# Optimization experiments

Measured on AMD Instinct MI355X. Metric: run time of the kernel, lower is better.

## Reference

```python
import jax, jax.numpy as jnp
import numpy as np

VOCAB, HID, LSTM_H, T_LEN, N_LAB, BATCH = 21128, 768, 128, 256, 9, 32


def _gru_dir(x, Wih, Whh, bih, bhh):
    # x: [B,T,D]; PyTorch GRU gate order: reset, update, new
    xp = jnp.einsum('btd,gd->tbg', x, Wih) + bih  # [T,B,3H]
    H = Whh.shape[1]
    def step(h, xt):
        gh = h @ Whh.T + bhh
        xr, xz, xn = jnp.split(xt, 3, axis=-1)
        hr, hz, hn = jnp.split(gh, 3, axis=-1)
        r = jax.nn.sigmoid(xr + hr)
        z = jax.nn.sigmoid(xz + hz)
        n = jnp.tanh(xn + r * hn)
        hnew = (1.0 - z) * n + z * h
        return hnew, hnew
    h0 = jnp.zeros((x.shape[0], H), x.dtype)
    _, hs = jax.lax.scan(step, h0, xp)
    return hs  # [T,B,H]


def _crf_llh(emissions, labels, trans, start, end):
    # emissions [B,T,L], labels [B,T]; full mask (all ones)
    e = jnp.transpose(emissions, (1, 0, 2))  # [T,B,L]
    emit_scores = jnp.take_along_axis(e, labels.T[:, :, None], axis=2)[:, :, 0]  # [T,B]
    trans_scores = trans[labels[:, :-1], labels[:, 1:]]  # [B,T-1]
    num = start[labels[:, 0]] + emit_scores.sum(0) + trans_scores.sum(1) + end[labels[:, -1]]
    def step(alpha, et):
        alpha = jax.nn.logsumexp(alpha[:, :, None] + trans[None] + et[:, None, :], axis=1)
        return alpha, None
    alpha0 = start + e[0]
    alpha, _ = jax.lax.scan(step, alpha0, e[1:])
    denom = jax.nn.logsumexp(alpha + end, axis=1)
    return num - denom  # [B]


def _viterbi(emissions, trans, start, end):
    e = jnp.transpose(emissions, (1, 0, 2))  # [T,B,L]
    def step(alpha, et):
        scores = alpha[:, :, None] + trans[None]  # [B,L_prev,L_cur]
        bp = jnp.argmax(scores, axis=1)
        alpha = jnp.max(scores, axis=1) + et
        return alpha, bp
    alpha0 = start + e[0]
    alpha, bps = jax.lax.scan(step, alpha0, e[1:])  # bps: [T-1,B,L]
    last = jnp.argmax(alpha + end, axis=1)  # [B]
    def back(y, bp):
        yprev = jnp.take_along_axis(bp, y[:, None], axis=1)[:, 0]
        return yprev, yprev
    _, path = jax.lax.scan(back, last, bps, reverse=True)  # [T-1,B]
    return jnp.concatenate([path, last[None]], axis=0).T  # [B,T]


def setup_inputs() -> dict:
    key = jax.random.key(0)
    ks = jax.random.split(key, 16)
    s = 0.02
    inp = {
        'input_ids': jax.random.randint(ks[0], (BATCH, T_LEN), 0, VOCAB),
        'attention_mask': jnp.ones((BATCH, T_LEN), jnp.int64 if jax.config.jax_enable_x64 else jnp.int32),
        'labels': jax.random.randint(ks[1], (BATCH, T_LEN), 0, N_LAB),
        'emb': jax.random.normal(ks[2], (VOCAB, HID), jnp.float32) * s,
        'Wih_f': jax.random.normal(ks[3], (3 * LSTM_H, HID), jnp.float32) * s,
        'Whh_f': jax.random.normal(ks[4], (3 * LSTM_H, LSTM_H), jnp.float32) * s,
        'bih_f': jnp.zeros((3 * LSTM_H,), jnp.float32),
        'bhh_f': jnp.zeros((3 * LSTM_H,), jnp.float32),
        'Wih_b': jax.random.normal(ks[5], (3 * LSTM_H, HID), jnp.float32) * s,
        'Whh_b': jax.random.normal(ks[6], (3 * LSTM_H, LSTM_H), jnp.float32) * s,
        'bih_b': jnp.zeros((3 * LSTM_H,), jnp.float32),
        'bhh_b': jnp.zeros((3 * LSTM_H,), jnp.float32),
        'Wlin': jax.random.normal(ks[7], (N_LAB, 2 * LSTM_H), jnp.float32) * s,
        'blin': jnp.zeros((N_LAB,), jnp.float32),
        'trans': jax.random.normal(ks[8], (N_LAB, N_LAB), jnp.float32) * 0.1,
        'start': jax.random.normal(ks[9], (N_LAB,), jnp.float32) * 0.1,
        'end': jax.random.normal(ks[10], (N_LAB,), jnp.float32) * 0.1,
    }
    return inp


def reference(input_ids, attention_mask, labels, emb, Wih_f, Whh_f, bih_f, bhh_f,
              Wih_b, Whh_b, bih_b, bhh_b, Wlin, blin, trans, start, end):
    x = emb[input_ids]  # [B,T,HID]
    hf = _gru_dir(x, Wih_f, Whh_f, bih_f, bhh_f)                 # [T,B,H]
    hb = _gru_dir(x[:, ::-1, :], Wih_b, Whh_b, bih_b, bhh_b)[::-1]  # [T,B,H]
    seq = jnp.concatenate([hf, hb], axis=-1).transpose(1, 0, 2)  # [B,T,2H]
    emissions = seq @ Wlin.T + blin                              # [B,T,L]
    decoded = _viterbi(emissions, trans, start, end)             # [B,T] int
    llh = _crf_llh(emissions, labels, trans, start, end)         # [B]
    loss = -jnp.mean(llh)
    return decoded, loss
```

## Files before the change

### kernel.cpp

```cpp
#include <hip/hip_runtime.h>
#include <math.h>

#define T_LEN 256
#define BATCH 32
#define HID   768
#define GH    384
#define LH    128
#define NLAB  9
#define M_TOT (T_LEN*BATCH)

typedef float v2f __attribute__((ext_vector_type(2)));
typedef _Float16 h8 __attribute__((ext_vector_type(8)));
typedef float f4 __attribute__((ext_vector_type(4)));

#define BC(x, i) __int_as_float(__builtin_amdgcn_ds_swizzle(__float_as_int(x), (i) << 5))

#define BAR_LGKM() do {                                   \
    asm volatile("s_waitcnt lgkmcnt(0)" ::: "memory");    \
    __builtin_amdgcn_s_barrier();                         \
    asm volatile("" ::: "memory");                        \
  } while (0)

__global__ __launch_bounds__(256, 2) void k_gemm_xp(
    const int* __restrict__ ids, const float* __restrict__ emb,
    const float* __restrict__ Wf, const float* __restrict__ Wb,
    const float* __restrict__ bihf, const float* __restrict__ bihb,
    float* __restrict__ xp)
{
  __shared__ __align__(16) _Float16 Ah[128*40];
  __shared__ __align__(16) _Float16 Bh[128*40];

  const int tid  = threadIdx.x;
  const int lane = tid & 63, w = tid >> 6;
  const int m0 = blockIdx.y * 128, n0 = blockIdx.x * 128;

  const int srow = tid >> 1, sk = (tid & 1) * 16;
  const int gm = m0 + srow;
  const int tok = ids[(gm & 31) * T_LEN + (gm >> 5)];
  const float* aG = emb + (size_t)tok * HID + sk;
  const int gn = n0 + srow;
  const float* bG = (gn < GH ? Wf + (size_t)gn * HID
                             : Wb + (size_t)(gn - GH) * HID) + sk;

  const int fr = lane & 15, fq = lane >> 4;
  const int mrow = (w & 1) * 64;
  const int ncol = (w >> 1) * 64;

  f4 acc[4][4];
#pragma unroll
  for (int i = 0; i < 4; ++i)
#pragma unroll
    for (int j = 0; j < 4; ++j) acc[i][j] = f4{0,0,0,0};

  const int sb = srow * 40 + sk;

  float4 ra[4], rb[4];
#pragma unroll
  for (int c = 0; c < 4; ++c) {
    ra[c] = *reinterpret_cast<const float4*>(aG + 4 * c);
    rb[c] = *reinterpret_cast<const float4*>(bG + 4 * c);
  }

  for (int kt = 0; kt < HID / 32; ++kt) {
    BAR_LGKM();
#pragma unroll
    for (int m = 0; m < 2; ++m) {
      const float4* src = m ? rb : ra;
      _Float16* dsth = m ? Bh : Ah;
#pragma unroll
      for (int seg = 0; seg < 2; ++seg) {
        float xs[8] = {src[2*seg].x, src[2*seg].y, src[2*seg].z, src[2*seg].w,
                       src[2*seg+1].x, src[2*seg+1].y, src[2*seg+1].z, src[2*seg+1].w};
        h8 hi;
#pragma unroll
        for (int c = 0; c < 8; ++c) hi[c] = (_Float16)xs[c];
        *reinterpret_cast<h8*>(&dsth[sb + seg * 8]) = hi;
      }
    }
    if (kt + 1 < HID / 32) {
      const float* pa = aG + (kt + 1) * 32;
      const float* pb = bG + (kt + 1) * 32;
#pragma unroll
      for (int c = 0; c < 4; ++c) {
        ra[c] = *reinterpret_cast<const float4*>(pa + 4 * c);
        rb[c] = *reinterpret_cast<const float4*>(pb + 4 * c);
      }
    }
    BAR_LGKM();

    h8 fbh[4];
#pragma unroll
    for (int j = 0; j < 4; ++j) {
      const int off = (ncol + j * 16 + fr) * 40 + fq * 8;
      fbh[j] = *reinterpret_cast<const h8*>(&Bh[off]);
    }
#pragma unroll
    for (int i = 0; i < 4; ++i) {
      const int off = (mrow + i * 16 + fr) * 40 + fq * 8;
      h8 fah = *reinterpret_cast<const h8*>(&Ah[off]);
#pragma unroll
      for (int j = 0; j < 4; ++j)
        acc[i][j] = __builtin_amdgcn_mfma_f32_16x16x32_f16(fah, fbh[j], acc[i][j], 0, 0, 0);
    }
  }

  float bcol[4];
#pragma unroll
  for (int j = 0; j < 4; ++j) {
    const int c = n0 + ncol + j * 16 + fr;
    bcol[j] = (c < GH) ? bihf[c] : bihb[c - GH];
  }
#pragma unroll
  for (int i = 0; i < 4; ++i)
#pragma unroll
    for (int j = 0; j < 4; ++j) {
      const int col = n0 + ncol + j * 16 + fr;
#pragma unroll
      for (int r = 0; r < 4; ++r) {
        const int row = m0 + mrow + i * 16 + fq * 4 + r;
        xp[(size_t)row * HID + col] = acc[i][j][r] + bcol[j];
      }
    }
}

__global__ __attribute__((amdgpu_flat_work_group_size(512, 512),
                          amdgpu_waves_per_eu(2, 2)))
void k_gru(
    const float* __restrict__ xp,
    const float* __restrict__ Whhf, const float* __restrict__ Whhb,
    const float* __restrict__ bhhf, const float* __restrict__ bhhb,
    float* __restrict__ hbuf, float* __restrict__ lossp)
{
  __shared__ __align__(1024) _Float16 hsp[2][256];
  const int tid = threadIdx.x;
  const int g   = tid >> 2;
  const int q   = tid & 3;
  const int bd  = blockIdx.x;
  const int dir = bd >> 5, b = bd & 31;
  const float* Whh = dir ? Whhb : Whhf;
  const float* bhh = dir ? bhhb : bhhf;

  if (bd == 0 && tid == 0) *lossp = 0.f;

  const float br = bhh[g], bz = bhh[g + LH], bn = bhh[g + 2*LH];
  const float* wg0 = Whh + (size_t)(0*LH + g) * LH + q * 32;
  const float* wg1 = Whh + (size_t)(1*LH + g) * LH + q * 32;
  const float* wg2 = Whh + (size_t)(2*LH + g) * LH + q * 32;

  const int t0 = dir ? (T_LEN - 1) : 0;
  const int dt = dir ? -1 : 1;
  const float* px = xp + (size_t)t0 * BATCH * HID + b * HID + dir * GH + g;
  float*       ph = hbuf + (size_t)t0 * BATCH * 256 + b * 256 + dir * LH + g;

  const long long xs = (long long)dt * BATCH * HID * 4;
  const long long hs = (long long)dt * BATCH * 256 * 4;
  const unsigned xslo = (unsigned)(xs & 0xffffffffll);
  const int      xshi = (int)(xs >> 32);
  const unsigned hslo = (unsigned)(hs & 0xffffffffll);
  const int      hshi = (int)(hs >> 32);
  const unsigned xlo = (unsigned)(uintptr_t)px, xhi = (unsigned)((uintptr_t)px >> 32);
  const unsigned hlo = (unsigned)(uintptr_t)ph, hhi = (unsigned)((uintptr_t)ph >> 32);
  const unsigned rd0 = (unsigned)(uintptr_t)(&hsp[0][q * 32]);
  const unsigned wr0 = (unsigned)(uintptr_t)(&hsp[1][g]);

  if (tid < 128) reinterpret_cast<unsigned*>(&hsp[0][0])[tid] = 0u;
  BAR_LGKM();

  int cnt = T_LEN;
  asm volatile(
    "global_load_dwordx4 v[128:131], %[wg0], off\n\t"
    "global_load_dwordx4 v[132:135], %[wg0], off offset:16\n\t"
    "global_load_dwordx4 v[136:139], %[wg0], off offset:32\n\t"
    "global_load_dwordx4 v[140:143], %[wg0], off offset:48\n\t"
    "global_load_dwordx4 v[144:147], %[wg0], off offset:64\n\t"
    "global_load_dwordx4 v[148:151], %[wg0], off offset:80\n\t"
    "global_load_dwordx4 v[152:155], %[wg0], off offset:96\n\t"
    "global_load_dwordx4 v[156:159], %[wg0], off offset:112\n\t"
    "global_load_dwordx4 v[160:163], %[wg1], off\n\t"
    "global_load_dwordx4 v[164:167], %[wg1], off offset:16\n\t"
    "global_load_dwordx4 v[168:171], %[wg1], off offset:32\n\t"
    "global_load_dwordx4 v[172:175], %[wg1], off offset:48\n\t"
    "global_load_dwordx4 v[176:179], %[wg1], off offset:64\n\t"
    "global_load_dwordx4 v[180:183], %[wg1], off offset:80\n\t"
    "global_load_dwordx4 v[184:187], %[wg1], off offset:96\n\t"
    "global_load_dwordx4 v[188:191], %[wg1], off offset:112\n\t"
    "global_load_dwordx4 v[192:195], %[wg2], off\n\t"
    "global_load_dwordx4 v[196:199], %[wg2], off offset:16\n\t"
    "global_load_dwordx4 v[200:203], %[wg2], off offset:32\n\t"
    "global_load_dwordx4 v[204:207], %[wg2], off offset:48\n\t"
    "global_load_dwordx4 v[208:211], %[wg2], off offset:64\n\t"
    "global_load_dwordx4 v[212:215], %[wg2], off offset:80\n\t"
    "global_load_dwordx4 v[216:219], %[wg2], off offset:96\n\t"
    "global_load_dwordx4 v[220:223], %[wg2], off offset:112\n\t"
    "v_mov_b32 v96, %[xlo]\n\t"
    "v_mov_b32 v97, %[xhi]\n\t"
    "v_mov_b32 v98, %[hlo]\n\t"
    "v_mov_b32 v99, %[hhi]\n\t"
    "v_mov_b32 v100, %[rd0]\n\t"
    "v_mov_b32 v101, %[wr0]\n\t"
    "global_load_dword v107, v[96:97], off\n\t"
    "global_load_dword v108, v[96:97], off offset:512\n\t"
    "global_load_dword v109, v[96:97], off offset:1024\n\t"
    "s_waitcnt vmcnt(3)\n\t"
    "v_cvt_pkrtz_f16_f32 v128, v128, v129\n\t"
    "v_cvt_pkrtz_f16_f32 v129, v130, v131\n\t"
    "v_cvt_pkrtz_f16_f32 v130, v132, v133\n\t"
    "v_cvt_pkrtz_f16_f32 v131, v134, v135\n\t"
    "v_cvt_pkrtz_f16_f32 v132, v136, v137\n\t"
    "v_cvt_pkrtz_f16_f32 v133, v138, v139\n\t"
    "v_cvt_pkrtz_f16_f32 v134, v140, v141\n\t"
    "v_cvt_pkrtz_f16_f32 v135, v142, v143\n\t"
    "v_cvt_pkrtz_f16_f32 v136, v144, v145\n\t"
    "v_cvt_pkrtz_f16_f32 v137, v146, v147\n\t"
    "v_cvt_pkrtz_f16_f32 v138, v148, v149\n\t"
    "v_cvt_pkrtz_f16_f32 v139, v150, v151\n\t"
    "v_cvt_pkrtz_f16_f32 v140, v152, v153\n\t"
    "v_cvt_pkrtz_f16_f32 v141, v154, v155\n\t"
    "v_cvt_pkrtz_f16_f32 v142, v156, v157\n\t"
    "v_cvt_pkrtz_f16_f32 v143, v158, v159\n\t"
    "v_cvt_pkrtz_f16_f32 v144, v160, v161\n\t"
    "v_cvt_pkrtz_f16_f32 v145, v162, v163\n\t"
    "v_cvt_pkrtz_f16_f32 v146, v164, v165\n\t"
    "v_cvt_pkrtz_f16_f32 v147, v166, v167\n\t"
    "v_cvt_pkrtz_f16_f32 v148, v168, v169\n\t"
    "v_cvt_pkrtz_f16_f32 v149, v170, v171\n\t"
    "v_cvt_pkrtz_f16_f32 v150, v172, v173\n\t"
    "v_cvt_pkrtz_f16_f32 v151, v174, v175\n\t"
    "v_cvt_pkrtz_f16_f32 v152, v176, v177\n\t"
    "v_cvt_pkrtz_f16_f32 v153, v178, v179\n\t"
    "v_cvt_pkrtz_f16_f32 v154, v180, v181\n\t"
    "v_cvt_pkrtz_f16_f32 v155, v182, v183\n\t"
    "v_cvt_pkrtz_f16_f32 v156, v184, v185\n\t"
    "v_cvt_pkrtz_f16_f32 v157, v186, v187\n\t"
    "v_cvt_pkrtz_f16_f32 v158, v188, v189\n\t"
    "v_cvt_pkrtz_f16_f32 v159, v190, v191\n\t"
    "v_cvt_pkrtz_f16_f32 v160, v192, v193\n\t"
    "v_cvt_pkrtz_f16_f32 v161, v194, v195\n\t"
    "v_cvt_pkrtz_f16_f32 v162, v196, v197\n\t"
    "v_cvt_pkrtz_f16_f32 v163, v198, v199\n\t"
    "v_cvt_pkrtz_f16_f32 v164, v200, v201\n\t"
    "v_cvt_pkrtz_f16_f32 v165, v202, v203\n\t"
    "v_cvt_pkrtz_f16_f32 v166, v204, v205\n\t"
    "v_cvt_pkrtz_f16_f32 v167, v206, v207\n\t"
    "v_cvt_pkrtz_f16_f32 v168, v208, v209\n\t"
    "v_cvt_pkrtz_f16_f32 v169, v210, v211\n\t"
    "v_cvt_pkrtz_f16_f32 v170, v212, v213\n\t"
    "v_cvt_pkrtz_f16_f32 v171, v214, v215\n\t"
    "v_cvt_pkrtz_f16_f32 v172, v216, v217\n\t"
    "v_cvt_pkrtz_f16_f32 v173, v218, v219\n\t"
    "v_cvt_pkrtz_f16_f32 v174, v220, v221\n\t"
    "v_cvt_pkrtz_f16_f32 v175, v222, v223\n\t"
    "v_mov_b32 v110, 0\n\t"
    "s_waitcnt vmcnt(0)\n\t"
    "0:\n\t"
    "s_waitcnt vmcnt(1)\n\t"
    "v_mov_b32 v104, v107\n\t"
    "v_mov_b32 v105, v108\n\t"
    "v_mov_b32 v106, v109\n\t"
    "ds_read_b128 v[176:179], v100\n\t"
    "ds_read_b128 v[180:183], v100 offset:16\n\t"
    "ds_read_b128 v[184:187], v100 offset:32\n\t"
    "ds_read_b128 v[188:191], v100 offset:48\n\t"
    "s_cmp_gt_u32 %[cnt], 1\n\t"
    "s_cbranch_scc0 3f\n\t"
    "v_add_co_u32 v96, vcc, %[xslo], v96\n\t"
    "v_addc_co_u32 v97, vcc, %[xshi], v97, vcc\n\t"
    "3:\n\t"
    "global_load_dword v107, v[96:97], off\n\t"
    "global_load_dword v108, v[96:97], off offset:512\n\t"
    "global_load_dword v109, v[96:97], off offset:1024\n\t"
    "s_waitcnt lgkmcnt(0)\n\t"
    "v_mov_b32 v116, 0\n\t"
    "v_mov_b32 v117, 0\n\t"
    "v_mov_b32 v118, 0\n\t"
    "v_mov_b32 v119, 0\n\t"
    "v_mov_b32 v120, 0\n\t"
    "v_mov_b32 v121, 0\n\t"
    "v_dot2_f32_f16 v116, v128, v176, v116\n\t"
    "v_dot2_f32_f16 v118, v144, v176, v118\n\t"
    "v_dot2_f32_f16 v120, v160, v176, v120\n\t"
    "v_dot2_f32_f16 v117, v129, v177, v117\n\t"
    "v_dot2_f32_f16 v119, v145, v177, v119\n\t"
    "v_dot2_f32_f16 v121, v161, v177, v121\n\t"
    "v_dot2_f32_f16 v116, v130, v178, v116\n\t"
    "v_dot2_f32_f16 v118, v146, v178, v118\n\t"
    "v_dot2_f32_f16 v120, v162, v178, v120\n\t"
    "v_dot2_f32_f16 v117, v131, v179, v117\n\t"
    "v_dot2_f32_f16 v119, v147, v179, v119\n\t"
    "v_dot2_f32_f16 v121, v163, v179, v121\n\t"
    "v_dot2_f32_f16 v116, v132, v180, v116\n\t"
    "v_dot2_f32_f16 v118, v148, v180, v118\n\t"
    "v_dot2_f32_f16 v120, v164, v180, v120\n\t"
    "v_dot2_f32_f16 v117, v133, v181, v117\n\t"
    "v_dot2_f32_f16 v119, v149, v181, v119\n\t"
    "v_dot2_f32_f16 v121, v165, v181, v121\n\t"
    "v_dot2_f32_f16 v116, v134, v182, v116\n\t"
    "v_dot2_f32_f16 v118, v150, v182, v118\n\t"
    "v_dot2_f32_f16 v120, v166, v182, v120\n\t"
    "v_dot2_f32_f16 v117, v135, v183, v117\n\t"
    "v_dot2_f32_f16 v119, v151, v183, v119\n\t"
    "v_dot2_f32_f16 v121, v167, v183, v121\n\t"
    "v_dot2_f32_f16 v116, v136, v184, v116\n\t"
    "v_dot2_f32_f16 v118, v152, v184, v118\n\t"
    "v_dot2_f32_f16 v120, v168, v184, v120\n\t"
    "v_dot2_f32_f16 v117, v137, v185, v117\n\t"
    "v_dot2_f32_f16 v119, v153, v185, v119\n\t"
    "v_dot2_f32_f16 v121, v169, v185, v121\n\t"
    "v_dot2_f32_f16 v116, v138, v186, v116\n\t"
    "v_dot2_f32_f16 v118, v154, v186, v118\n\t"
    "v_dot2_f32_f16 v120, v170, v186, v120\n\t"
    "v_dot2_f32_f16 v117, v139, v187, v117\n\t"
    "v_dot2_f32_f16 v119, v155, v187, v119\n\t"
    "v_dot2_f32_f16 v121, v171, v187, v121\n\t"
    "v_dot2_f32_f16 v116, v140, v188, v116\n\t"
    "v_dot2_f32_f16 v118, v156, v188, v118\n\t"
    "v_dot2_f32_f16 v120, v172, v188, v120\n\t"
    "v_dot2_f32_f16 v117, v141, v189, v117\n\t"
    "v_dot2_f32_f16 v119, v157, v189, v119\n\t"
    "v_dot2_f32_f16 v121, v173, v189, v121\n\t"
    "v_dot2_f32_f16 v116, v142, v190, v116\n\t"
    "v_dot2_f32_f16 v118, v158, v190, v118\n\t"
    "v_dot2_f32_f16 v120, v174, v190, v120\n\t"
    "v_dot2_f32_f16 v117, v143, v191, v117\n\t"
    "v_dot2_f32_f16 v119, v159, v191, v119\n\t"
    "v_dot2_f32_f16 v121, v175, v191, v121\n\t"
    "v_add_f32 v116, v116, v117\n\t"
    "v_add_f32 v118, v118, v119\n\t"
    "v_add_f32 v120, v120, v121\n\t"
    "s_nop 1\n\t"
    "v_add_f32 v116, v116, v116 quad_perm:[1,0,3,2] row_mask:0xf bank_mask:0xf\n\t"
    "v_add_f32 v118, v118, v118 quad_perm:[1,0,3,2] row_mask:0xf bank_mask:0xf\n\t"
    "v_add_f32 v120, v120, v120 quad_perm:[1,0,3,2] row_mask:0xf bank_mask:0xf\n\t"
    "s_nop 1\n\t"
    "v_add_f32 v116, v116, v116 quad_perm:[2,3,0,1] row_mask:0xf bank_mask:0xf\n\t"
    "v_add_f32 v118, v118, v118 quad_perm:[2,3,0,1] row_mask:0xf bank_mask:0xf\n\t"
    "v_add_f32 v120, v120, v120 quad_perm:[2,3,0,1] row_mask:0xf bank_mask:0xf\n\t"
    "s_nop 1\n\t"
    "v_add_f32 v111, v104, v116\n\t"
    "v_add_f32 v112, v105, v118\n\t"
    "v_add_f32 v113, v120, %[bn]\n\t"
    "v_add_f32 v111, v111, %[br]\n\t"
    "v_add_f32 v112, v112, %[bz]\n\t"
    "v_mul_f32 v111, 0xbfb8aa3b, v111\n\t"
    "v_mul_f32 v112, 0xbfb8aa3b, v112\n\t"
    "v_exp_f32 v111, v111\n\t"
    "v_exp_f32 v112, v112\n\t"
    "s_nop 0\n\t"
    "v_add_f32 v111, 1.0, v111\n\t"
    "v_add_f32 v112, 1.0, v112\n\t"
    "v_rcp_f32 v111, v111\n\t"
    "v_rcp_f32 v112, v112\n\t"
    "s_nop 0\n\t"
    "v_fmac_f32 v106, v111, v113\n\t"
    "v_mul_f32 v113, 0x4038aa3b, v106\n\t"
    "v_exp_f32 v113, v113\n\t"
    "v_sub_f32 v115, 1.0, v112\n\t"
    "s_nop 0\n\t"
    "v_add_f32 v114, -1.0, v113\n\t"
    "v_add_f32 v113, 1.0, v113\n\t"
    "v_rcp_f32 v113, v113\n\t"
    "s_nop 1\n\t"
    "v_mul_f32 v114, v114, v113\n\t"
    "v_mul_f32 v115, v115, v114\n\t"
    "v_fmac_f32 v115, v112, v110\n\t"
    "v_mov_b32 v110, v115\n\t"
    "v_cvt_f16_f32 v114, v115\n\t"
    "global_store_dword v[98:99], v115, off\n\t"
    "v_add_co_u32 v98, vcc, %[hslo], v98\n\t"
    "v_addc_co_u32 v99, vcc, %[hshi], v99, vcc\n\t"
    "ds_write_b16 v101, v114\n\t"
    "v_xor_b32 v100, 0x200, v100\n\t"
    "v_xor_b32 v101, 0x200, v101\n\t"
    "s_waitcnt lgkmcnt(0)\n\t"
    "s_barrier\n\t"
    "s_sub_u32 %[cnt], %[cnt], 1\n\t"
    "s_cmp_lg_u32 %[cnt], 0\n\t"
    "s_cbranch_scc1 0b\n\t"
    : [cnt]"+s"(cnt)
    : [wg0]"v"(wg0), [wg1]"v"(wg1), [wg2]"v"(wg2),
      [xlo]"v"(xlo), [xhi]"v"(xhi), [hlo]"v"(hlo), [hhi]"v"(hhi),
      [rd0]"v"(rd0), [wr0]"v"(wr0),
      [br]"v"(br), [bz]"v"(bz), [bn]"v"(bn),
      [xslo]"s"(xslo), [xshi]"v"(xshi), [hslo]"s"(hslo), [hshi]"v"(hshi)
    : "memory", "vcc", "scc",
      "v96","v97","v98","v99","v100","v101","v102","v103","v104","v105",
      "v106","v107","v108","v109","v110","v111","v112","v113","v114","v115",
      "v116","v117","v118","v119","v120","v121","v122","v123","v124","v125",
      "v126","v127","v128","v129","v130","v131","v132","v133","v134","v135",
      "v136","v137","v138","v139","v140","v141","v142","v143","v144","v145",
      "v146","v147","v148","v149","v150","v151","v152","v153","v154","v155",
      "v156","v157","v158","v159","v160","v161","v162","v163","v164","v165",
      "v166","v167","v168","v169","v170","v171","v172","v173","v174","v175",
      "v176","v177","v178","v179","v180","v181","v182","v183","v184","v185",
      "v186","v187","v188","v189","v190","v191","v192","v193","v194","v195",
      "v196","v197","v198","v199","v200","v201","v202","v203","v204","v205",
      "v206","v207","v208","v209","v210","v211","v212","v213","v214","v215",
      "v216","v217","v218","v219","v220","v221","v222","v223");
}

__global__ __launch_bounds__(256, 1) void k_crf_fused(
    const float* __restrict__ hbuf, const float* __restrict__ Wlin,
    const float* __restrict__ blin, const int* __restrict__ labels,
    const float* __restrict__ trans, const float* __restrict__ start,
    const float* __restrict__ endv, float* __restrict__ dec_out,
    float* __restrict__ lossp)
{
  __shared__ float el[T_LEN * 10];
  __shared__ __align__(16) unsigned char bp8[(T_LEN - 1) * 16];
  const int b    = blockIdx.x;
  const int tid  = threadIdx.x;
  const int lane = tid & 63, w = tid >> 6;
  const int sub  = lane >> 4, l16 = lane & 15;

  float4 wreg[NLAB][4];
#pragma unroll
  for (int j = 0; j < NLAB; ++j)
#pragma unroll
    for (int c = 0; c < 4; ++c)
      wreg[j][c] = *reinterpret_cast<const float4*>(Wlin + j * 256 + l16 * 16 + c * 4);

  for (int k = 0; k < 16; ++k) {
    const int t = w * 64 + k * 4 + sub;
    const float* hp = hbuf + ((size_t)t * BATCH + b) * 256 + l16 * 16;
    const float4 h0 = *reinterpret_cast<const float4*>(hp);
    const float4 h1 = *reinterpret_cast<const float4*>(hp + 4);
    const float4 h2 = *reinterpret_cast<const float4*>(hp + 8);
    const float4 h3 = *reinterpret_cast<const float4*>(hp + 12);
    float acc[NLAB];
#pragma unroll
    for (int j = 0; j < NLAB; ++j) {
      const float4 w0 = wreg[j][0], w1 = wreg[j][1], w2 = wreg[j][2], w3 = wreg[j][3];
      float s0 = h0.x*w0.x + h0.y*w0.y + h0.z*w0.z + h0.w*w0.w;
      float s1 = h1.x*w1.x + h1.y*w1.y + h1.z*w1.z + h1.w*w1.w;
      float s2 = h2.x*w2.x + h2.y*w2.y + h2.z*w2.z + h2.w*w2.w;
      float s3 = h3.x*w3.x + h3.y*w3.y + h3.z*w3.z + h3.w*w3.w;
      acc[j] = (s0 + s1) + (s2 + s3);
    }
#pragma unroll
    for (int j = 0; j < NLAB; ++j) {
#pragma unroll
      for (int off = 1; off < 16; off <<= 1)
        acc[j] += __shfl_xor(acc[j], off);
    }
    if (l16 < NLAB) {
      float v = acc[0];
#pragma unroll
      for (int j = 1; j < NLAB; ++j) v = (l16 == j) ? acc[j] : v;
      el[t * 10 + l16] = v + blin[l16];
    }
  }
  __syncthreads();

  if (w == 0) {
    float tcol[NLAB];
#pragma unroll
    for (int i = 0; i < NLAB; ++i)
      tcol[i] = (lane < NLAB) ? trans[i * NLAB + lane] : 0.f;
    float alpha = (lane < NLAB) ? (start[lane] + el[lane]) : -3e38f;
    float et_next = (lane < NLAB) ? el[10 + lane] : 0.f;
    for (int s = 0; s < T_LEN - 1; ++s) {
      const float et = et_next;
      if (s < T_LEN - 2)
        et_next = (lane < NLAB) ? el[(s + 2) * 10 + lane] : 0.f;
      float v[NLAB];
      v[0] = BC(alpha, 0) + tcol[0];
      v[1] = BC(alpha, 1) + tcol[1];
      v[2] = BC(alpha, 2) + tcol[2];
      v[3] = BC(alpha, 3) + tcol[3];
      v[4] = BC(alpha, 4) + tcol[4];
      v[5] = BC(alpha, 5) + tcol[5];
      v[6] = BC(alpha, 6) + tcol[6];
      v[7] = BC(alpha, 7) + tcol[7];
      v[8] = BC(alpha, 8) + tcol[8];
      float v01 = (v[0] >= v[1]) ? v[0] : v[1];  int i01 = (v[0] >= v[1]) ? 0 : 1;
      float v23 = (v[2] >= v[3]) ? v[2] : v[3];  int i23 = (v[2] >= v[3]) ? 2 : 3;
      float v45 = (v[4] >= v[5]) ? v[4] : v[5];  int i45 = (v[4] >= v[5]) ? 4 : 5;
      float v67 = (v[6] >= v[7]) ? v[6] : v[7];  int i67 = (v[6] >= v[7]) ? 6 : 7;
      float va = (v01 >= v23) ? v01 : v23;       int ia = (v01 >= v23) ? i01 : i23;
      float vb = (v45 >= v67) ? v45 : v67;       int ib = (v45 >= v67) ? i45 : i67;
      float vc = (va >= vb) ? va : vb;           int ic = (va >= vb) ? ia : ib;
      float best = (vc >= v[8]) ? vc : v[8];     int bi = (vc >= v[8]) ? ic : 8;
      alpha = best + et;
      if (lane < NLAB) bp8[s * 16 + lane] = (unsigned char)bi;
    }
    float fin = alpha + ((lane < NLAB) ? endv[lane] : 0.f);
    float fv[NLAB];
    fv[0] = BC(fin, 0); fv[1] = BC(fin, 1); fv[2] = BC(fin, 2);
    fv[3] = BC(fin, 3); fv[4] = BC(fin, 4); fv[5] = BC(fin, 5);
    fv[6] = BC(fin, 6); fv[7] = BC(fin, 7); fv[8] = BC(fin, 8);
    float f01 = (fv[0] >= fv[1]) ? fv[0] : fv[1];  int j01 = (fv[0] >= fv[1]) ? 0 : 1;
    float f23 = (fv[2] >= fv[3]) ? fv[2] : fv[3];  int j23 = (fv[2] >= fv[3]) ? 2 : 3;
    float f45 = (fv[4] >= fv[5]) ? fv[4] : fv[5];  int j45 = (fv[4] >= fv[5]) ? 4 : 5;
    float f67 = (fv[6] >= fv[7]) ? fv[6] : fv[7];  int j67 = (fv[6] >= fv[7]) ? 6 : 7;
    float fa = (f01 >= f23) ? f01 : f23;           int ja = (f01 >= f23) ? j01 : j23;
    float fb = (f45 >= f67) ? f45 : f67;           int jb = (f45 >= f67) ? j45 : j67;
    float fc = (fa >= fb) ? fa : fb;               int jc = (fa >= fb) ? ja : jb;
    int last = (fc >= fv[8]) ? jc : 8;
    if (lane == 0) {
      int y = last;
      dec_out[b * T_LEN + (T_LEN - 1)] = (float)y;
      uint4 row = *reinterpret_cast<const uint4*>(&bp8[(T_LEN - 2) * 16]);
      for (int s = T_LEN - 2; s >= 0; --s) {
        uint4 nrow = row;
        if (s > 0) nrow = *reinterpret_cast<const uint4*>(&bp8[(s - 1) * 16]);
        unsigned wsel = (y < 4) ? row.x : ((y < 8) ? row.y : row.z);
        y = (int)((wsel >> ((y & 3) * 8)) & 0xffu);
        dec_out[b * T_LEN + s] = (float)y;
        row = nrow;
      }
    }
  } else if (w == 1) {
    float tcol[NLAB];
#pragma unroll
    for (int i = 0; i < NLAB; ++i)
      tcol[i] = (lane < NLAB) ? trans[i * NLAB + lane] : 0.f;
    float ca = (lane < NLAB) ? (start[lane] + el[lane]) : -3e38f;
    float et_next = (lane < NLAB) ? el[10 + lane] : 0.f;
    for (int s = 0; s < T_LEN - 1; ++s) {
      const float et = et_next;
      if (s < T_LEN - 2)
        et_next = (lane < NLAB) ? el[(s + 2) * 10 + lane] : 0.f;
      float c[NLAB];
      c[0] = BC(ca, 0) + tcol[0];
      c[1] = BC(ca, 1) + tcol[1];
      c[2] = BC(ca, 2) + tcol[2];
      c[3] = BC(ca, 3) + tcol[3];
      c[4] = BC(ca, 4) + tcol[4];
      c[5] = BC(ca, 5) + tcol[5];
      c[6] = BC(ca, 6) + tcol[6];
      c[7] = BC(ca, 7) + tcol[7];
      c[8] = BC(ca, 8) + tcol[8];
      float m01 = fmaxf(c[0], c[1]), m23 = fmaxf(c[2], c[3]);
      float m45 = fmaxf(c[4], c[5]), m67 = fmaxf(c[6], c[7]);
      float m = fmaxf(fmaxf(fmaxf(m01, m23), fmaxf(m45, m67)), c[8]);
      float p0 = __expf(c[0]-m) + __expf(c[1]-m), p1 = __expf(c[2]-m) + __expf(c[3]-m);
      float p2 = __expf(c[4]-m) + __expf(c[5]-m), p3 = __expf(c[6]-m) + __expf(c[7]-m);
      float p = ((p0 + p1) + (p2 + p3)) + __expf(c[8]-m);
      ca = m + __logf(p) + et;
    }
    float fv[NLAB];
    fv[0] = BC(ca, 0) + endv[0];
    fv[1] = BC(ca, 1) + endv[1];
    fv[2] = BC(ca, 2) + endv[2];
    fv[3] = BC(ca, 3) + endv[3];
    fv[4] = BC(ca, 4) + endv[4];
    fv[5] = BC(ca, 5) + endv[5];
    fv[6] = BC(ca, 6) + endv[6];
    fv[7] = BC(ca, 7) + endv[7];
    fv[8] = BC(ca, 8) + endv[8];
    float mx = -3e38f;
#pragma unroll
    for (int j = 0; j < NLAB; ++j) mx = fmaxf(mx, fv[j]);
    float ps = 0.f;
#pragma unroll
    for (int j = 0; j < NLAB; ++j) ps += __expf(fv[j] - mx);
    float denom = mx + __logf(ps);

    const int* lb = labels + b * T_LEN;
    float part = 0.f;
    for (int t4 = 0; t4 < 4; ++t4) {
      int t = lane * 4 + t4;
      int l = lb[t];
      part += el[t * 10 + l];
      if (t > 0) part += trans[lb[t - 1] * NLAB + l];
    }
#pragma unroll
    for (int off = 32; off > 0; off >>= 1) part += __shfl_xor(part, off);
    if (lane == 0) {
      float num = part + start[lb[0]] + endv[lb[T_LEN - 1]];
      float llh = num - denom;
      atomicAdd(lossp, -llh * (1.0f / BATCH));
    }
  }
}

extern "C" void kernel_launch(void* const* d_in, const int* in_sizes, int n_in,
                              void* d_out, int out_size, void* d_ws, size_t ws_size,
                              hipStream_t stream) {
  const int*   ids    = (const int*)d_in[0];
  const int*   labels = (const int*)d_in[2];
  const float* emb    = (const float*)d_in[3];
  const float* Wihf   = (const float*)d_in[4];
  const float* Whhf   = (const float*)d_in[5];
  const float* bihf   = (const float*)d_in[6];
  const float* bhhf   = (const float*)d_in[7];
  const float* Wihb   = (const float*)d_in[8];
  const float* Whhb   = (const float*)d_in[9];
  const float* bihb   = (const float*)d_in[10];
  const float* bhhb   = (const float*)d_in[11];
  const float* Wlin   = (const float*)d_in[12];
  const float* blin   = (const float*)d_in[13];
  const float* trans  = (const float*)d_in[14];
  const float* start  = (const float*)d_in[15];
  const float* endv   = (const float*)d_in[16];

  float* xp    = (float*)d_ws;
  float* hbuf  = xp + (size_t)M_TOT * HID;
  float* out   = (float*)d_out;
  float* lossp = out + M_TOT;

  k_gemm_xp<<<dim3(6, 64), 256, 0, stream>>>(ids, emb, Wihf, Wihb, bihf, bihb, xp);
  k_gru<<<64, 512, 0, stream>>>(xp, Whhf, Whhb, bhhf, bhhb, hbuf, lossp);
  k_crf_fused<<<BATCH, 256, 0, stream>>>(hbuf, Wlin, blin, labels, trans,
                                         start, endv, out, lossp);
}
```

Measured before the change: 360.0 us.

## Split GRU hidden-row dot products across two lanes instead of four

The recurrent GRU kernel now uses 256 threads per block, with two lanes per hidden unit, each holding 64 columns of the three Whh gate rows in fp16 registers instead of 32. Each lane reads 128 bytes of h from LDS per step and one cross-lane DPP reduction stage is removed. The aim is to shorten the per-timestep critical path by using fewer waves, fewer barrier participants and a shallower reduction. The cost is twice the dot-product work per lane and a register footprint that reaches v255.

After: 355.1 us. About the same (-1.4%).

```diff
diff --git a/kernel.cpp b/kernel.cpp
--- a/kernel.cpp
+++ b/kernel.cpp
@@ -123,8 +123,8 @@
     }
 }
 
-__global__ __attribute__((amdgpu_flat_work_group_size(512, 512),
-                          amdgpu_waves_per_eu(2, 2)))
+__global__ __attribute__((amdgpu_flat_work_group_size(256, 256),
+                          amdgpu_waves_per_eu(1, 1)))
 void k_gru(
     const float* __restrict__ xp,
     const float* __restrict__ Whhf, const float* __restrict__ Whhb,
@@ -133,8 +133,8 @@
 {
   __shared__ __align__(1024) _Float16 hsp[2][256];
   const int tid = threadIdx.x;
-  const int g   = tid >> 2;
-  const int q   = tid & 3;
+  const int g   = tid >> 1;
+  const int hf  = tid & 1;
   const int bd  = blockIdx.x;
   const int dir = bd >> 5, b = bd & 31;
   const float* Whh = dir ? Whhb : Whhf;
@@ -143,9 +143,9 @@
   if (bd == 0 && tid == 0) *lossp = 0.f;
 
   const float br = bhh[g], bz = bhh[g + LH], bn = bhh[g + 2*LH];
-  const float* wg0 = Whh + (size_t)(0*LH + g) * LH + q * 32;
-  const float* wg1 = Whh + (size_t)(1*LH + g) * LH + q * 32;
-  const float* wg2 = Whh + (size_t)(2*LH + g) * LH + q * 32;
+  const float* wg0 = Whh + (size_t)(0*LH + g) * LH + hf * 64;
+  const float* wg1 = Whh + (size_t)(1*LH + g) * LH + hf * 64;
+  const float* wg2 = Whh + (size_t)(2*LH + g) * LH + hf * 64;
 
   const int t0 = dir ? (T_LEN - 1) : 0;
   const int dt = dir ? -1 : 1;
@@ -160,7 +160,7 @@
   const int      hshi = (int)(hs >> 32);
   const unsigned xlo = (unsigned)(uintptr_t)px, xhi = (unsigned)((uintptr_t)px >> 32);
   const unsigned hlo = (unsigned)(uintptr_t)ph, hhi = (unsigned)((uintptr_t)ph >> 32);
-  const unsigned rd0 = (unsigned)(uintptr_t)(&hsp[0][q * 32]);
+  const unsigned rd0 = (unsigned)(uintptr_t)(&hsp[0][hf * 64]);
   const unsigned wr0 = (unsigned)(uintptr_t)(&hsp[1][g]);
 
   if (tid < 128) reinterpret_cast<unsigned*>(&hsp[0][0])[tid] = 0u;
@@ -176,32 +176,37 @@
     "global_load_dwordx4 v[148:151], %[wg0], off offset:80\n\t"
     "global_load_dwordx4 v[152:155], %[wg0], off offset:96\n\t"
     "global_load_dwordx4 v[156:159], %[wg0], off offset:112\n\t"
-    "global_load_dwordx4 v[160:163], %[wg1], off\n\t"
-    "global_load_dwordx4 v[164:167], %[wg1], off offset:16\n\t"
-    "global_load_dwordx4 v[168:171], %[wg1], off offset:32\n\t"
-    "global_load_dwordx4 v[172:175], %[wg1], off offset:48\n\t"
-    "global_load_dwordx4 v[176:179], %[wg1], off offset:64\n\t"
-    "global_load_dwordx4 v[180:183], %[wg1], off offset:80\n\t"
-    "global_load_dwordx4 v[184:187], %[wg1], off offset:96\n\t"
-    "global_load_dwordx4 v[188:191], %[wg1], off offset:112\n\t"
-    "global_load_dwordx4 v[192:195], %[wg2], off\n\t"
-    "global_load_dwordx4 v[196:199], %[wg2], off offset:16\n\t"
-    "global_load_dwordx4 v[200:203], %[wg2], off offset:32\n\t"
-    "global_load_dwordx4 v[204:207], %[wg2], off offset:48\n\t"
-    "global_load_dwordx4 v[208:211], %[wg2], off offset:64\n\t"
-    "global_load_dwordx4 v[212:215], %[wg2], off offset:80\n\t"
-    "global_load_dwordx4 v[216:219], %[wg2], off offset:96\n\t"
-    "global_load_dwordx4 v[220:223], %[wg2], off offset:112\n\t"
+    "global_load_dwordx4 v[160:163], %[wg0], off offset:128\n\t"
+    "global_load_dwordx4 v[164:167], %[wg0], off offset:144\n\t"
+    "global_load_dwordx4 v[168:171], %[wg0], off offset:160\n\t"
+    "global_load_dwordx4 v[172:175], %[wg0], off offset:176\n\t"
+    "global_load_dwordx4 v[176:179], %[wg0], off offset:192\n\t"
+    "global_load_dwordx4 v[180:183], %[wg0], off offset:208\n\t"
+    "global_load_dwordx4 v[184:187], %[wg0], off offset:224\n\t"
+    "global_load_dwordx4 v[188:191], %[wg0], off offset:240\n\t"
+    "global_load_dwordx4 v[192:195], %[wg1], off\n\t"
+    "global_load_dwordx4 v[196:199], %[wg1], off offset:16\n\t"
+    "global_load_dwordx4 v[200:203], %[wg1], off offset:32\n\t"
+    "global_load_dwordx4 v[204:207], %[wg1], off offset:48\n\t"
+    "global_load_dwordx4 v[208:211], %[wg1], off offset:64\n\t"
+    "global_load_dwordx4 v[212:215], %[wg1], off offset:80\n\t"
+    "global_load_dwordx4 v[216:219], %[wg1], off offset:96\n\t"
+    "global_load_dwordx4 v[220:223], %[wg1], off offset:112\n\t"
+    "global_load_dwordx4 v[224:227], %[wg1], off offset:128\n\t"
+    "global_load_dwordx4 v[228:231], %[wg1], off offset:144\n\t"
+    "global_load_dwordx4 v[232:235], %[wg1], off offset:160\n\t"
+    "global_load_dwordx4 v[236:239], %[wg1], off offset:176\n\t"
+    "global_load_dwordx4 v[240:243], %[wg1], off offset:192\n\t"
+    "global_load_dwordx4 v[244:247], %[wg1], off offset:208\n\t"
+    "global_load_dwordx4 v[248:251], %[wg1], off offset:224\n\t"
+    "global_load_dwordx4 v[252:255], %[wg1], off offset:240\n\t"
     "v_mov_b32 v96, %[xlo]\n\t"
     "v_mov_b32 v97, %[xhi]\n\t"
     "v_mov_b32 v98, %[hlo]\n\t"
     "v_mov_b32 v99, %[hhi]\n\t"
     "v_mov_b32 v100, %[rd0]\n\t"
     "v_mov_b32 v101, %[wr0]\n\t"
-    "global_load_dword v107, v[96:97], off\n\t"
-    "global_load_dword v108, v[96:97], off offset:512\n\t"
-    "global_load_dword v109, v[96:97], off offset:1024\n\t"
-    "s_waitcnt vmcnt(3)\n\t"
+    "s_waitcnt vmcnt(0)\n\t"
     "v_cvt_pkrtz_f16_f32 v128, v128, v129\n\t"
     "v_cvt_pkrtz_f16_f32 v129, v130, v131\n\t"
     "v_cvt_pkrtz_f16_f32 v130, v132, v133\n\t"
@@ -250,6 +255,74 @@
     "v_cvt_pkrtz_f16_f32 v173, v218, v219\n\t"
     "v_cvt_pkrtz_f16_f32 v174, v220, v221\n\t"
     "v_cvt_pkrtz_f16_f32 v175, v222, v223\n\t"
+    "v_cvt_pkrtz_f16_f32 v176, v224, v225\n\t"
+    "v_cvt_pkrtz_f16_f32 v177, v226, v227\n\t"
+    "v_cvt_pkrtz_f16_f32 v178, v228, v229\n\t"
+    "v_cvt_pkrtz_f16_f32 v179, v230, v231\n\t"
+    "v_cvt_pkrtz_f16_f32 v180, v232, v233\n\t"
+    "v_cvt_pkrtz_f16_f32 v181, v234, v235\n\t"
+    "v_cvt_pkrtz_f16_f32 v182, v236, v237\n\t"
+    "v_cvt_pkrtz_f16_f32 v183, v238, v239\n\t"
+    "v_cvt_pkrtz_f16_f32 v184, v240, v241\n\t"
+    "v_cvt_pkrtz_f16_f32 v185, v242, v243\n\t"
+    "v_cvt_pkrtz_f16_f32 v186, v244, v245\n\t"
+    "v_cvt_pkrtz_f16_f32 v187, v246, v247\n\t"
+    "v_cvt_pkrtz_f16_f32 v188, v248, v249\n\t"
+    "v_cvt_pkrtz_f16_f32 v189, v250, v251\n\t"
+    "v_cvt_pkrtz_f16_f32 v190, v252, v253\n\t"
+    "v_cvt_pkrtz_f16_f32 v191, v254, v255\n\t"
+    "global_load_dwordx4 v[192:195], %[wg2], off\n\t"
+    "global_load_dwordx4 v[196:199], %[wg2], off offset:16\n\t"
+    "global_load_dwordx4 v[200:203], %[wg2], off offset:32\n\t"
+    "global_load_dwordx4 v[204:207], %[wg2], off offset:48\n\t"
+    "global_load_dwordx4 v[208:211], %[wg2], off offset:64\n\t"
+    "global_load_dwordx4 v[212:215], %[wg2], off offset:80\n\t"
+    "global_load_dwordx4 v[216:219], %[wg2], off offset:96\n\t"
+    "global_load_dwordx4 v[220:223], %[wg2], off offset:112\n\t"
+    "global_load_dwordx4 v[224:227], %[wg2], off offset:128\n\t"
+    "global_load_dwordx4 v[228:231], %[wg2], off offset:144\n\t"
+    "global_load_dwordx4 v[232:235], %[wg2], off offset:160\n\t"
+    "global_load_dwordx4 v[236:239], %[wg2], off offset:176\n\t"
+    "global_load_dwordx4 v[240:243], %[wg2], off offset:192\n\t"
+    "global_load_dwordx4 v[244:247], %[wg2], off offset:208\n\t"
+    "global_load_dwordx4 v[248:251], %[wg2], off offset:224\n\t"
+    "global_load_dwordx4 v[252:255], %[wg2], off offset:240\n\t"
+    "global_load_dword v107, v[96:97], off\n\t"
+    "global_load_dword v108, v[96:97], off offset:512\n\t"
+    "global_load_dword v109, v[96:97], off offset:1024\n\t"
+    "s_waitcnt vmcnt(3)\n\t"
+    "v_cvt_pkrtz_f16_f32 v192, v192, v193\n\t"
+    "v_cvt_pkrtz_f16_f32 v193, v194, v195\n\t"
+    "v_cvt_pkrtz_f16_f32 v194, v196, v197\n\t"
+    "v_cvt_pkrtz_f16_f32 v195, v198, v199\n\t"
+    "v_cvt_pkrtz_f16_f32 v196, v200, v201\n\t"
+    "v_cvt_pkrtz_f16_f32 v197, v202, v203\n\t"
+    "v_cvt_pkrtz_f16_f32 v198, v204, v205\n\t"
+    "v_cvt_pkrtz_f16_f32 v199, v206, v207\n\t"
+    "v_cvt_pkrtz_f16_f32 v200, v208, v209\n\t"
+    "v_cvt_pkrtz_f16_f32 v201, v210, v211\n\t"
+    "v_cvt_pkrtz_f16_f32 v202, v212, v213\n\t"
+    "v_cvt_pkrtz_f16_f32 v203, v214, v215\n\t"
+    "v_cvt_pkrtz_f16_f32 v204, v216, v217\n\t"
+    "v_cvt_pkrtz_f16_f32 v205, v218, v219\n\t"
+    "v_cvt_pkrtz_f16_f32 v206, v220, v221\n\t"
+    "v_cvt_pkrtz_f16_f32 v207, v222, v223\n\t"
+    "v_cvt_pkrtz_f16_f32 v208, v224, v225\n\t"
+    "v_cvt_pkrtz_f16_f32 v209, v226, v227\n\t"
+    "v_cvt_pkrtz_f16_f32 v210, v228, v229\n\t"
+    "v_cvt_pkrtz_f16_f32 v211, v230, v231\n\t"
+    "v_cvt_pkrtz_f16_f32 v212, v232, v233\n\t"
+    "v_cvt_pkrtz_f16_f32 v213, v234, v235\n\t"
+    "v_cvt_pkrtz_f16_f32 v214, v236, v237\n\t"
+    "v_cvt_pkrtz_f16_f32 v215, v238, v239\n\t"
+    "v_cvt_pkrtz_f16_f32 v216, v240, v241\n\t"
+    "v_cvt_pkrtz_f16_f32 v217, v242, v243\n\t"
+    "v_cvt_pkrtz_f16_f32 v218, v244, v245\n\t"
+    "v_cvt_pkrtz_f16_f32 v219, v246, v247\n\t"
+    "v_cvt_pkrtz_f16_f32 v220, v248, v249\n\t"
+    "v_cvt_pkrtz_f16_f32 v221, v250, v251\n\t"
+    "v_cvt_pkrtz_f16_f32 v222, v252, v253\n\t"
+    "v_cvt_pkrtz_f16_f32 v223, v254, v255\n\t"
     "v_mov_b32 v110, 0\n\t"
     "s_waitcnt vmcnt(0)\n\t"
     "0:\n\t"
@@ -257,10 +330,14 @@
     "v_mov_b32 v104, v107\n\t"
     "v_mov_b32 v105, v108\n\t"
     "v_mov_b32 v106, v109\n\t"
-    "ds_read_b128 v[176:179], v100\n\t"
-    "ds_read_b128 v[180:183], v100 offset:16\n\t"
-    "ds_read_b128 v[184:187], v100 offset:32\n\t"
-    "ds_read_b128 v[188:191], v100 offset:48\n\t"
+    "ds_read_b128 v[224:227], v100\n\t"
+    "ds_read_b128 v[228:231], v100 offset:16\n\t"
+    "ds_read_b128 v[232:235], v100 offset:32\n\t"
+    "ds_read_b128 v[236:239], v100 offset:48\n\t"
+    "ds_read_b128 v[240:243], v100 offset:64\n\t"
+    "ds_read_b128 v[244:247], v100 offset:80\n\t"
+    "ds_read_b128 v[248:251], v100 offset:96\n\t"
+    "ds_read_b128 v[252:255], v100 offset:112\n\t"
     "s_cmp_gt_u32 %[cnt], 1\n\t"
     "s_cbranch_scc0 3f\n\t"
     "v_add_co_u32 v96, vcc, %[xslo], v96\n\t"
@@ -276,54 +353,102 @@
     "v_mov_b32 v119, 0\n\t"
     "v_mov_b32 v120, 0\n\t"
     "v_mov_b32 v121, 0\n\t"
-    "v_dot2_f32_f16 v116, v128, v176, v116\n\t"
-    "v_dot2_f32_f16 v118, v144, v176, v118\n\t"
-    "v_dot2_f32_f16 v120, v160, v176, v120\n\t"
-    "v_dot2_f32_f16 v117, v129, v177, v117\n\t"
-    "v_dot2_f32_f16 v119, v145, v177, v119\n\t"
-    "v_dot2_f32_f16 v121, v161, v177, v121\n\t"
-    "v_dot2_f32_f16 v116, v130, v178, v116\n\t"
-    "v_dot2_f32_f16 v118, v146, v178, v118\n\t"
-    "v_dot2_f32_f16 v120, v162, v178, v120\n\t"
-    "v_dot2_f32_f16 v117, v131, v179, v117\n\t"
-    "v_dot2_f32_f16 v119, v147, v179, v119\n\t"
-    "v_dot2_f32_f16 v121, v163, v179, v121\n\t"
-    "v_dot2_f32_f16 v116, v132, v180, v116\n\t"
-    "v_dot2_f32_f16 v118, v148, v180, v118\n\t"
-    "v_dot2_f32_f16 v120, v164, v180, v120\n\t"
-    "v_dot2_f32_f16 v117, v133, v181, v117\n\t"
-    "v_dot2_f32_f16 v119, v149, v181, v119\n\t"
-    "v_dot2_f32_f16 v121, v165, v181, v121\n\t"
-    "v_dot2_f32_f16 v116, v134, v182, v116\n\t"
-    "v_dot2_f32_f16 v118, v150, v182, v118\n\t"
-    "v_dot2_f32_f16 v120, v166, v182, v120\n\t"
-    "v_dot2_f32_f16 v117, v135, v183, v117\n\t"
-    "v_dot2_f32_f16 v119, v151, v183, v119\n\t"
-    "v_dot2_f32_f16 v121, v167, v183, v121\n\t"
-    "v_dot2_f32_f16 v116, v136, v184, v116\n\t"
-    "v_dot2_f32_f16 v118, v152, v184, v118\n\t"
-    "v_dot2_f32_f16 v120, v168, v184, v120\n\t"
-    "v_dot2_f32_f16 v117, v137, v185, v117\n\t"
-    "v_dot2_f32_f16 v119, v153, v185, v119\n\t"
-    "v_dot2_f32_f16 v121, v169, v185, v121\n\t"
-    "v_dot2_f32_f16 v116, v138, v186, v116\n\t"
-    "v_dot2_f32_f16 v118, v154, v186, v118\n\t"
-    "v_dot2_f32_f16 v120, v170, v186, v120\n\t"
-    "v_dot2_f32_f16 v117, v139, v187, v117\n\t"
-    "v_dot2_f32_f16 v119, v155, v187, v119\n\t"
-    "v_dot2_f32_f16 v121, v171, v187, v121\n\t"
-    "v_dot2_f32_f16 v116, v140, v188, v116\n\t"
-    "v_dot2_f32_f16 v118, v156, v188, v118\n\t"
-    "v_dot2_f32_f16 v120, v172, v188, v120\n\t"
-    "v_dot2_f32_f16 v117, v141, v189, v117\n\t"
-    "v_dot2_f32_f16 v119, v157, v189, v119\n\t"
-    "v_dot2_f32_f16 v121, v173, v189, v121\n\t"
-    "v_dot2_f32_f16 v116, v142, v190, v116\n\t"
-    "v_dot2_f32_f16 v118, v158, v190, v118\n\t"
-    "v_dot2_f32_f16 v120, v174, v190, v120\n\t"
-    "v_dot2_f32_f16 v117, v143, v191, v117\n\t"
-    "v_dot2_f32_f16 v119, v159, v191, v119\n\t"
-    "v_dot2_f32_f16 v121, v175, v191, v121\n\t"
+    "v_dot2_f32_f16 v116, v128, v224, v116\n\t"
+    "v_dot2_f32_f16 v118, v160, v224, v118\n\t"
+    "v_dot2_f32_f16 v120, v192, v224, v120\n\t"
+    "v_dot2_f32_f16 v117, v129, v225, v117\n\t"
+    "v_dot2_f32_f16 v119, v161, v225, v119\n\t"
+    "v_dot2_f32_f16 v121, v193, v225, v121\n\t"
+    "v_dot2_f32_f16 v116, v130, v226, v116\n\t"
+    "v_dot2_f32_f16 v118, v162, v226, v118\n\t"
+    "v_dot2_f32_f16 v120, v194, v226, v120\n\t"
+    "v_dot2_f32_f16 v117, v131, v227, v117\n\t"
+    "v_dot2_f32_f16 v119, v163, v227, v119\n\t"
+    "v_dot2_f32_f16 v121, v195, v227, v121\n\t"
+    "v_dot2_f32_f16 v116, v132, v228, v116\n\t"
+    "v_dot2_f32_f16 v118, v164, v228, v118\n\t"
+    "v_dot2_f32_f16 v120, v196, v228, v120\n\t"
+    "v_dot2_f32_f16 v117, v133, v229, v117\n\t"
+    "v_dot2_f32_f16 v119, v165, v229, v119\n\t"
+    "v_dot2_f32_f16 v121, v197, v229, v121\n\t"
+    "v_dot2_f32_f16 v116, v134, v230, v116\n\t"
+    "v_dot2_f32_f16 v118, v166, v230, v118\n\t"
+    "v_dot2_f32_f16 v120, v198, v230, v120\n\t"
+    "v_dot2_f32_f16 v117, v135, v231, v117\n\t"
+    "v_dot2_f32_f16 v119, v167, v231, v119\n\t"
+    "v_dot2_f32_f16 v121, v199, v231, v121\n\t"
+    "v_dot2_f32_f16 v116, v136, v232, v116\n\t"
+    "v_dot2_f32_f16 v118, v168, v232, v118\n\t"
+    "v_dot2_f32_f16 v120, v200, v232, v120\n\t"
+    "v_dot2_f32_f16 v117, v137, v233, v117\n\t"
+    "v_dot2_f32_f16 v119, v169, v233, v119\n\t"
+    "v_dot2_f32_f16 v121, v201, v233, v121\n\t"
+    "v_dot2_f32_f16 v116, v138, v234, v116\n\t"
+    "v_dot2_f32_f16 v118, v170, v234, v118\n\t"
+    "v_dot2_f32_f16 v120, v202, v234, v120\n\t"
+    "v_dot2_f32_f16 v117, v139, v235, v117\n\t"
+    "v_dot2_f32_f16 v119, v171, v235, v119\n\t"
+    "v_dot2_f32_f16 v121, v203, v235, v121\n\t"
+    "v_dot2_f32_f16 v116, v140, v236, v116\n\t"
+    "v_dot2_f32_f16 v118, v172, v236, v118\n\t"
+    "v_dot2_f32_f16 v120, v204, v236, v120\n\t"
+    "v_dot2_f32_f16 v117, v141, v237, v117\n\t"
+    "v_dot2_f32_f16 v119, v173, v237, v119\n\t"
+    "v_dot2_f32_f16 v121, v205, v237, v121\n\t"
+    "v_dot2_f32_f16 v116, v142, v238, v116\n\t"
+    "v_dot2_f32_f16 v118, v174, v238, v118\n\t"
+    "v_dot2_f32_f16 v120, v206, v238, v120\n\t"
+    "v_dot2_f32_f16 v117, v143, v239, v117\n\t"
+    "v_dot2_f32_f16 v119, v175, v239, v119\n\t"
+    "v_dot2_f32_f16 v121, v207, v239, v121\n\t"
+    "v_dot2_f32_f16 v116, v144, v240, v116\n\t"
+    "v_dot2_f32_f16 v118, v176, v240, v118\n\t"
+    "v_dot2_f32_f16 v120, v208, v240, v120\n\t"
+    "v_dot2_f32_f16 v117, v145, v241, v117\n\t"
+    "v_dot2_f32_f16 v119, v177, v241, v119\n\t"
+    "v_dot2_f32_f16 v121, v209, v241, v121\n\t"
+    "v_dot2_f32_f16 v116, v146, v242, v116\n\t"
+    "v_dot2_f32_f16 v118, v178, v242, v118\n\t"
+    "v_dot2_f32_f16 v120, v210, v242, v120\n\t"
+    "v_dot2_f32_f16 v117, v147, v243, v117\n\t"
+    "v_dot2_f32_f16 v119, v179, v243, v119\n\t"
+    "v_dot2_f32_f16 v121, v211, v243, v121\n\t"
+    "v_dot2_f32_f16 v116, v148, v244, v116\n\t"
+    "v_dot2_f32_f16 v118, v180, v244, v118\n\t"
+    "v_dot2_f32_f16 v120, v212, v244, v120\n\t"
+    "v_dot2_f32_f16 v117, v149, v245, v117\n\t"
+    "v_dot2_f32_f16 v119, v181, v245, v119\n\t"
+    "v_dot2_f32_f16 v121, v213, v245, v121\n\t"
+    "v_dot2_f32_f16 v116, v150, v246, v116\n\t"
+    "v_dot2_f32_f16 v118, v182, v246, v118\n\t"
+    "v_dot2_f32_f16 v120, v214, v246, v120\n\t"
+    "v_dot2_f32_f16 v117, v151, v247, v117\n\t"
+    "v_dot2_f32_f16 v119, v183, v247, v119\n\t"
+    "v_dot2_f32_f16 v121, v215, v247, v121\n\t"
+    "v_dot2_f32_f16 v116, v152, v248, v116\n\t"
+    "v_dot2_f32_f16 v118, v184, v248, v118\n\t"
+    "v_dot2_f32_f16 v120, v216, v248, v120\n\t"
+    "v_dot2_f32_f16 v117, v153, v249, v117\n\t"
+    "v_dot2_f32_f16 v119, v185, v249, v119\n\t"
+    "v_dot2_f32_f16 v121, v217, v249, v121\n\t"
+    "v_dot2_f32_f16 v116, v154, v250, v116\n\t"
+    "v_dot2_f32_f16 v118, v186, v250, v118\n\t"
+    "v_dot2_f32_f16 v120, v218, v250, v120\n\t"
+    "v_dot2_f32_f16 v117, v155, v251, v117\n\t"
+    "v_dot2_f32_f16 v119, v187, v251, v119\n\t"
+    "v_dot2_f32_f16 v121, v219, v251, v121\n\t"
+    "v_dot2_f32_f16 v116, v156, v252, v116\n\t"
+    "v_dot2_f32_f16 v118, v188, v252, v118\n\t"
+    "v_dot2_f32_f16 v120, v220, v252, v120\n\t"
+    "v_dot2_f32_f16 v117, v157, v253, v117\n\t"
+    "v_dot2_f32_f16 v119, v189, v253, v119\n\t"
+    "v_dot2_f32_f16 v121, v221, v253, v121\n\t"
+    "v_dot2_f32_f16 v116, v158, v254, v116\n\t"
+    "v_dot2_f32_f16 v118, v190, v254, v118\n\t"
+    "v_dot2_f32_f16 v120, v222, v254, v120\n\t"
+    "v_dot2_f32_f16 v117, v159, v255, v117\n\t"
+    "v_dot2_f32_f16 v119, v191, v255, v119\n\t"
+    "v_dot2_f32_f16 v121, v223, v255, v121\n\t"
     "v_add_f32 v116, v116, v117\n\t"
     "v_add_f32 v118, v118, v119\n\t"
     "v_add_f32 v120, v120, v121\n\t"
@@ -331,10 +456,6 @@
     "v_add_f32 v116, v116, v116 quad_perm:[1,0,3,2] row_mask:0xf bank_mask:0xf\n\t"
     "v_add_f32 v118, v118, v118 quad_perm:[1,0,3,2] row_mask:0xf bank_mask:0xf\n\t"
     "v_add_f32 v120, v120, v120 quad_perm:[1,0,3,2] row_mask:0xf bank_mask:0xf\n\t"
-    "s_nop 1\n\t"
-    "v_add_f32 v116, v116, v116 quad_perm:[2,3,0,1] row_mask:0xf bank_mask:0xf\n\t"
-    "v_add_f32 v118, v118, v118 quad_perm:[2,3,0,1] row_mask:0xf bank_mask:0xf\n\t"
-    "v_add_f32 v120, v120, v120 quad_perm:[2,3,0,1] row_mask:0xf bank_mask:0xf\n\t"
     "s_nop 1\n\t"
     "v_add_f32 v111, v104, v116\n\t"
     "v_add_f32 v112, v105, v118\n\t"
@@ -395,7 +516,10 @@
       "v186","v187","v188","v189","v190","v191","v192","v193","v194","v195",
       "v196","v197","v198","v199","v200","v201","v202","v203","v204","v205",
       "v206","v207","v208","v209","v210","v211","v212","v213","v214","v215",
-      "v216","v217","v218","v219","v220","v221","v222","v223");
+      "v216","v217","v218","v219","v220","v221","v222","v223","v224","v225",
+      "v226","v227","v228","v229","v230","v231","v232","v233","v234","v235",
+      "v236","v237","v238","v239","v240","v241","v242","v243","v244","v245",
+      "v246","v247","v248","v249","v250","v251","v252","v253","v254","v255");
 }
 
 __global__ __launch_bounds__(256, 1) void k_crf_fused(
@@ -600,7 +724,7 @@
   float* lossp = out + M_TOT;
 
   k_gemm_xp<<<dim3(6, 64), 256, 0, stream>>>(ids, emb, Wihf, Wihb, bihf, bihb, xp);
-  k_gru<<<64, 512, 0, stream>>>(xp, Whhf, Whhb, bhhf, bhhb, hbuf, lossp);
+  k_gru<<<64, 256, 0, stream>>>(xp, Whhf, Whhb, bhhf, bhhb, hbuf, lossp);
   k_crf_fused<<<BATCH, 256, 0, stream>>>(hbuf, Wlin, blin, labels, trans,
                                          start, endv, out, lossp);
 }
```
